# Performance work log

Hardware: AMD Instinct MI355X
Metric: run time of the kernel (lower is better)

The kernel has to match this reference:

```python
import jax, jax.numpy as jnp
import numpy as np

N_SENTS, N_ENTS, BATCH, DIM, HEADS = 64, 16, 64, 512, 8


def setup_inputs() -> dict:
    key = jax.random.key(0)
    ks = jax.random.split(key, 10)
    se = N_SENTS * N_ENTS
    s = 0.02  # init scale for projection weights
    entities = jax.random.normal(ks[0], (se, BATCH, DIM), dtype=jnp.float32)
    query_param = jax.random.uniform(ks[1], (1, 1, DIM), jnp.float32, -1.0, 1.0)
    wq = jax.random.normal(ks[2], (DIM, DIM), jnp.float32) * s
    wk = jax.random.normal(ks[3], (DIM, DIM), jnp.float32) * s
    wv = jax.random.normal(ks[4], (DIM, DIM), jnp.float32) * s
    wo = jax.random.normal(ks[5], (DIM, DIM), jnp.float32) * s
    bq = jax.random.normal(ks[6], (DIM,), jnp.float32) * s
    bk = jax.random.normal(ks[7], (DIM,), jnp.float32) * s
    bv = jax.random.normal(ks[8], (DIM,), jnp.float32) * s
    bo = jax.random.normal(ks[9], (DIM,), jnp.float32) * s
    return {"entities": entities, "query_param": query_param,
            "wq": wq, "wk": wk, "wv": wv, "wo": wo,
            "bq": bq, "bk": bk, "bv": bv, "bo": bo,
            "n_sents": N_SENTS}


def reference(entities, query_param, wq, wk, wv, wo, bq, bk, bv, bo, n_sents):
    # entities: [n_sents*n_ents, batch, dim]
    se, b, d = entities.shape
    n_ents = se // n_sents
    h = HEADS
    hd = d // h

    # Learned single query broadcast to every (sentence, batch) slot.
    q_in = jnp.broadcast_to(query_param, (n_sents, b, d))
    q = q_in @ wq.T + bq            # [n_sents, b, d]
    k = entities @ wk.T + bk        # [se, b, d]
    v = entities @ wv.T + bv        # [se, b, d]

    # Split heads -> [b, h, len, hd]
    qh = q.reshape(n_sents, b, h, hd).transpose(1, 2, 0, 3)
    kh = k.reshape(se, b, h, hd).transpose(1, 2, 0, 3)
    vh = v.reshape(se, b, h, hd).transpose(1, 2, 0, 3)

    scale = jnp.asarray(1.0 / np.sqrt(hd), dtype=qh.dtype)
    scores = jnp.einsum('bhqd,bhkd->bhqk', qh, kh) * scale  # [b,h,n_sents,se]

    # Block-diagonal mask: query i attends only to keys [i*n_ents, (i+1)*n_ents)
    valid = (jnp.arange(se) // n_ents)[None, :] == jnp.arange(n_sents)[:, None]
    scores = jnp.where(valid[None, None], scores, jnp.finfo(scores.dtype).min)

    attn = jax.nn.softmax(scores, axis=-1)
    ctx = jnp.einsum('bhqk,bhkd->bhqd', attn, vh)            # [b,h,n_sents,hd]
    out = ctx.transpose(2, 0, 1, 3).reshape(n_sents, b, d)   # merge heads
    return out @ wo.T + bo                                   # [n_sents, b, d]
```

## Files before the change

kernel.cpp:

```cpp
#include <hip/hip_runtime.h>
#include <stdint.h>

#define HEADS 8
#define DIM   512
#define HD    64
#define NE    16
#define NS    64
#define NB    64

typedef short bf16x8 __attribute__((ext_vector_type(8)));
typedef float f32x4  __attribute__((ext_vector_type(4)));

__device__ __forceinline__ unsigned short f2bf(float f) {
    union { float f; uint32_t u; } v; v.f = f;
    uint32_t u = v.u;
    u += 0x7fffu + ((u >> 16) & 1u);
    return (unsigned short)(u >> 16);
}
__device__ __forceinline__ float bf2f(unsigned short b) {
    union { uint32_t u; float f; } v; v.u = ((uint32_t)b) << 16;
    return v.f;
}

__global__ __launch_bounds__(256) void k_qvec(
    const float* __restrict__ qp, const float* __restrict__ wq,
    const float* __restrict__ bq, float* __restrict__ qvec)
{
    __shared__ float red[32][9];
    const int t = threadIdx.x;
    const int dl = t >> 3, js = t & 7;
    const int d = blockIdx.x * 32 + dl;
    const float* w = wq + (size_t)d * DIM + js * 64;
    const float* q = qp + js * 64;
    float acc = 0.f;
    #pragma unroll 8
    for (int i = 0; i < 64; i++) acc += w[i] * q[i];
    red[dl][js] = acc;
    __syncthreads();
    if (t < 32) {
        float s = 0.f;
        #pragma unroll
        for (int j = 0; j < 8; j++) s += red[t][j];
        const int dd = blockIdx.x * 32 + t;
        qvec[dd] = s + bq[dd];
    }
}

__global__ __launch_bounds__(256) void k_uproj(
    const float* __restrict__ qvec, const float* __restrict__ wk,
    unsigned short* __restrict__ u_bf)
{
    const int h = blockIdx.x;
    const int t = threadIdx.x;
    if (h >= HEADS) {
        ((uint32_t*)u_bf)[h * 256 + t] = 0u;
        return;
    }
    __shared__ float qs[HD];
    if (t < HD) qs[t] = qvec[h * HD + t];
    __syncthreads();
    for (int c = t; c < DIM; c += 256) {
        const float* w = wk + (size_t)(h * HD) * DIM + c;
        float acc = 0.f;
        #pragma unroll 4
        for (int j = 0; j < HD; j++) acc += qs[j] * w[(size_t)j * DIM];
        u_bf[h * DIM + c] = f2bf(acc);
    }
}

__global__ __launch_bounds__(256) void k_attn(
    const float* __restrict__ ents, const unsigned short* __restrict__ u_bf,
    unsigned short* __restrict__ weighted)
{
    __shared__ unsigned short ent_bf[NE * DIM];
    __shared__ float attn_s[NE][16];
    const int t = threadIdx.x;
    const int bid = blockIdx.x;
    const int s = bid >> 6, b = bid & 63;

    {
        const int e = t >> 4, c = t & 15;
        const float* src = ents + ((size_t)(s * NE + e) * NB + b) * DIM;
        const uint32_t swz  = (uint32_t)((e & 7) << 4);
        const uint32_t rowb = (uint32_t)e * (DIM * 2);
        #pragma unroll
        for (int i = 0; i < 8; i++) {
            const int d0 = 4 * c + 64 * i;
            const float4 v = *(const float4*)(src + d0);
            ushort4 hv;
            hv.x = f2bf(v.x); hv.y = f2bf(v.y); hv.z = f2bf(v.z); hv.w = f2bf(v.w);
            *(ushort4*)((char*)ent_bf + ((rowb + (uint32_t)d0 * 2u) ^ swz)) = hv;
        }
    }
    __syncthreads();

    if (t < 64) {
        const int m = t & 15, g = t >> 4;
        const uint32_t aswz = (uint32_t)((m & 7) << 4);
        const uint32_t arow = (uint32_t)m * (DIM * 2);
        const unsigned short* urow = u_bf + m * DIM;
        f32x4 acc = {0.f, 0.f, 0.f, 0.f};
        #pragma unroll
        for (int kk = 0; kk < DIM; kk += 32) {
            const int kp = kk + g * 8;
            bf16x8 af = *(const bf16x8*)((const char*)ent_bf + ((arow + (uint32_t)kp * 2u) ^ aswz));
            bf16x8 bf = *(const bf16x8*)(urow + kp);
            acc = __builtin_amdgcn_mfma_f32_16x16x32_bf16(af, bf, acc, 0, 0, 0);
        }
        const float scale = 0.125f;
        float s0 = acc[0]*scale, s1 = acc[1]*scale, s2 = acc[2]*scale, s3 = acc[3]*scale;
        float mx = fmaxf(fmaxf(s0, s1), fmaxf(s2, s3));
        mx = fmaxf(mx, __shfl_xor(mx, 16));
        mx = fmaxf(mx, __shfl_xor(mx, 32));
        const float p0 = __expf(s0 - mx), p1 = __expf(s1 - mx);
        const float p2 = __expf(s2 - mx), p3 = __expf(s3 - mx);
        float sm = p0 + p1 + p2 + p3;
        sm += __shfl_xor(sm, 16);
        sm += __shfl_xor(sm, 32);
        const float inv = 1.f / sm;
        attn_s[4 * g + 0][m] = p0 * inv;
        attn_s[4 * g + 1][m] = p1 * inv;
        attn_s[4 * g + 2][m] = p2 * inv;
        attn_s[4 * g + 3][m] = p3 * inv;
    }
    __syncthreads();

    float wa[HEADS], wb[HEADS];
    #pragma unroll
    for (int h = 0; h < HEADS; h++) { wa[h] = 0.f; wb[h] = 0.f; }
    const int d0 = 2 * t;
    #pragma unroll
    for (int ee = 0; ee < NE; ee++) {
        const uint32_t off = (((uint32_t)(ee * DIM + d0)) * 2u) ^ ((uint32_t)((ee & 7) << 4));
        const uint32_t pr = *(const uint32_t*)((const char*)ent_bf + off);
        const float v0 = bf2f((unsigned short)(pr & 0xffffu));
        const float v1 = bf2f((unsigned short)(pr >> 16));
        const float4 a0 = *(const float4*)&attn_s[ee][0];
        const float4 a1 = *(const float4*)&attn_s[ee][4];
        wa[0] += a0.x * v0; wb[0] += a0.x * v1;
        wa[1] += a0.y * v0; wb[1] += a0.y * v1;
        wa[2] += a0.z * v0; wb[2] += a0.z * v1;
        wa[3] += a0.w * v0; wb[3] += a0.w * v1;
        wa[4] += a1.x * v0; wb[4] += a1.x * v1;
        wa[5] += a1.y * v0; wb[5] += a1.y * v1;
        wa[6] += a1.z * v0; wb[6] += a1.z * v1;
        wa[7] += a1.w * v0; wb[7] += a1.w * v1;
    }
    unsigned short* wrow = weighted + (size_t)bid * (HEADS * DIM);
    #pragma unroll
    for (int h = 0; h < HEADS; h++) {
        const uint32_t pk = (uint32_t)f2bf(wa[h]) | ((uint32_t)f2bf(wb[h]) << 16);
        *(uint32_t*)(wrow + h * DIM + d0) = pk;
    }
}

template <typename CT>
__global__ __launch_bounds__(256) void k_gemm(
    const unsigned short* __restrict__ A, int lda, int aOffY,
    const float* __restrict__ B, int ldb, int bOffY,
    const float* __restrict__ bias, CT* __restrict__ C, int ldc, int cOffY, int K)
{
    __shared__ unsigned short a_s[64][72];
    __shared__ unsigned short b_s[64][72];
    const int t = threadIdx.x;
    const int m0 = blockIdx.x * 64;
    const int y  = blockIdx.y;
    const int w = t >> 6, l = t & 63;
    const int m = l & 15, g = l >> 4;
    const int lr = t >> 2, lk = (t & 3) * 16;

    const unsigned short* Ap = A + (size_t)(m0 + lr) * lda + (size_t)aOffY * y;
    const float* Bp = B + (size_t)(bOffY * y + lr) * ldb;

    f32x4 acc[4];
    #pragma unroll
    for (int i = 0; i < 4; i++) acc[i] = (f32x4){0.f, 0.f, 0.f, 0.f};

    for (int k0 = 0; k0 < K; k0 += 64) {
        const ushort4 av0 = *(const ushort4*)(Ap + k0 + lk);
        const ushort4 av1 = *(const ushort4*)(Ap + k0 + lk + 4);
        const ushort4 av2 = *(const ushort4*)(Ap + k0 + lk + 8);
        const ushort4 av3 = *(const ushort4*)(Ap + k0 + lk + 12);
        const float4 bv0 = *(const float4*)(Bp + k0 + lk);
        const float4 bv1 = *(const float4*)(Bp + k0 + lk + 4);
        const float4 bv2 = *(const float4*)(Bp + k0 + lk + 8);
        const float4 bv3 = *(const float4*)(Bp + k0 + lk + 12);
        *(ushort4*)&a_s[lr][lk]      = av0;
        *(ushort4*)&a_s[lr][lk + 4]  = av1;
        *(ushort4*)&a_s[lr][lk + 8]  = av2;
        *(ushort4*)&a_s[lr][lk + 12] = av3;
        ushort4 h0, h1, h2, h3;
        h0.x = f2bf(bv0.x); h0.y = f2bf(bv0.y); h0.z = f2bf(bv0.z); h0.w = f2bf(bv0.w);
        h1.x = f2bf(bv1.x); h1.y = f2bf(bv1.y); h1.z = f2bf(bv1.z); h1.w = f2bf(bv1.w);
        h2.x = f2bf(bv2.x); h2.y = f2bf(bv2.y); h2.z = f2bf(bv2.z); h2.w = f2bf(bv2.w);
        h3.x = f2bf(bv3.x); h3.y = f2bf(bv3.y); h3.z = f2bf(bv3.z); h3.w = f2bf(bv3.w);
        *(ushort4*)&b_s[lr][lk]      = h0;
        *(ushort4*)&b_s[lr][lk + 4]  = h1;
        *(ushort4*)&b_s[lr][lk + 8]  = h2;
        *(ushort4*)&b_s[lr][lk + 12] = h3;
        __syncthreads();
        #pragma unroll
        for (int kk = 0; kk < 64; kk += 32) {
            const int kp = kk + g * 8;
            const bf16x8 af = *(const bf16x8*)&a_s[w * 16 + m][kp];
            const bf16x8 b0 = *(const bf16x8*)&b_s[ 0 + m][kp];
            const bf16x8 b1 = *(const bf16x8*)&b_s[16 + m][kp];
            const bf16x8 b2 = *(const bf16x8*)&b_s[32 + m][kp];
            const bf16x8 b3 = *(const bf16x8*)&b_s[48 + m][kp];
            acc[0] = __builtin_amdgcn_mfma_f32_16x16x32_bf16(af, b0, acc[0], 0, 0, 0);
            acc[1] = __builtin_amdgcn_mfma_f32_16x16x32_bf16(af, b1, acc[1], 0, 0, 0);
            acc[2] = __builtin_amdgcn_mfma_f32_16x16x32_bf16(af, b2, acc[2], 0, 0, 0);
            acc[3] = __builtin_amdgcn_mfma_f32_16x16x32_bf16(af, b3, acc[3], 0, 0, 0);
        }
        __syncthreads();
    }

    const int colbase = cOffY * y;
    #pragma unroll
    for (int nt = 0; nt < 4; nt++) {
        const int col = colbase + nt * 16 + m;
        const float bs = bias[col];
        #pragma unroll
        for (int j = 0; j < 4; j++) {
            const int row = m0 + w * 16 + g * 4 + j;
            const float val = acc[nt][j] + bs;
            if (sizeof(CT) == 2) {
                ((unsigned short*)C)[(size_t)row * ldc + col] = f2bf(val);
            } else {
                ((float*)C)[(size_t)row * ldc + col] = val;
            }
        }
    }
}

extern "C" void kernel_launch(void* const* d_in, const int* in_sizes, int n_in,
                              void* d_out, int out_size, void* d_ws, size_t ws_size,
                              hipStream_t stream)
{
    const float* ents = (const float*)d_in[0];
    const float* qp   = (const float*)d_in[1];
    const float* wq   = (const float*)d_in[2];
    const float* wk   = (const float*)d_in[3];
    const float* wv   = (const float*)d_in[4];
    const float* wo   = (const float*)d_in[5];
    const float* bq   = (const float*)d_in[6];
    const float* bv   = (const float*)d_in[8];
    const float* bo   = (const float*)d_in[9];

    char* ws = (char*)d_ws;
    float*          qvec     = (float*)ws;
    unsigned short* u_bf     = (unsigned short*)(ws + 2048);
    unsigned short* weighted = (unsigned short*)(ws + 32768);
    unsigned short* ctx      = (unsigned short*)(ws + 32768 + 33554432);

    k_qvec <<<16, 256, 0, stream>>>(qp, wq, bq, qvec);
    k_uproj<<<16, 256, 0, stream>>>(qvec, wk, u_bf);
    k_attn <<<4096, 256, 0, stream>>>(ents, u_bf, weighted);
    k_gemm<unsigned short><<<dim3(64, 8), 256, 0, stream>>>(
        weighted, HEADS * DIM, DIM, wv, DIM, HD, bv, ctx, DIM, HD, DIM);
    k_gemm<float><<<dim3(64, 8), 256, 0, stream>>>(
        ctx, DIM, 0, wo, DIM, HD, bo, (float*)d_out, DIM, HD, DIM);
}
```

Baseline: 74.67 us.

## Batch four batch slots per attention block and pre-convert weights to bf16

The attention kernel now processes four batch slots per block, so all four wavefronts run the score MFMA instead of one. Each thread also accumulates eight contiguous dims with 16-byte LDS reads and stores. The Wv/Wo fp32 weights are converted to bf16 once in a new prep kernel, removing per-tile conversion in the GEMMs. qvec and u projections are re-split into more, smaller blocks. Costs are a 64KB LDS footprint per attention block, which limits occupancy, and 64 accumulator registers per thread.

```diff
diff --git a/kernel.cpp b/kernel.cpp
--- a/kernel.cpp
+++ b/kernel.cpp
@@ -22,88 +22,100 @@
     return v.f;
 }
 
-__global__ __launch_bounds__(256) void k_qvec(
+__global__ __launch_bounds__(256) void k_prep(
     const float* __restrict__ qp, const float* __restrict__ wq,
-    const float* __restrict__ bq, float* __restrict__ qvec)
-{
-    __shared__ float red[32][9];
+    const float* __restrict__ bq, const float* __restrict__ wv,
+    const float* __restrict__ wo, float* __restrict__ qvec,
+    unsigned short* __restrict__ wv_bf, unsigned short* __restrict__ wo_bf)
+{
+    const int bid = blockIdx.x;
     const int t = threadIdx.x;
-    const int dl = t >> 3, js = t & 7;
-    const int d = blockIdx.x * 32 + dl;
-    const float* w = wq + (size_t)d * DIM + js * 64;
-    const float* q = qp + js * 64;
+    if (bid < 64) {
+        const int dl = t >> 5, js = t & 31;
+        const int d = bid * 8 + dl;
+        const float* w = wq + (size_t)d * DIM + js * 16;
+        const float* q = qp + js * 16;
+        float acc = 0.f;
+        #pragma unroll
+        for (int i = 0; i < 16; i++) acc += w[i] * q[i];
+        #pragma unroll
+        for (int msk = 16; msk >= 1; msk >>= 1) acc += __shfl_xor(acc, msk);
+        if (js == 0) qvec[d] = acc + bq[d];
+        return;
+    }
+    const bool is_v = bid < 320;
+    const float* src = is_v ? wv : wo;
+    unsigned short* dst = is_v ? wv_bf : wo_bf;
+    const int li = ((is_v ? bid - 64 : bid - 320) * 1024 + t * 4);
+    const float4 v = *(const float4*)(src + li);
+    ushort4 hv;
+    hv.x = f2bf(v.x); hv.y = f2bf(v.y); hv.z = f2bf(v.z); hv.w = f2bf(v.w);
+    *(ushort4*)(dst + li) = hv;
+}
+
+__global__ __launch_bounds__(64) void k_uproj(
+    const float* __restrict__ qvec, const float* __restrict__ wk,
+    unsigned short* __restrict__ u_bf)
+{
+    const int bid = blockIdx.x;
+    const int l = threadIdx.x;
+    if (bid >= 64) {
+        const int row = 8 + (bid - 64);
+        ((uint4*)(u_bf + row * DIM))[l & 63] = (uint4){0u, 0u, 0u, 0u};
+        return;
+    }
+    const int h = bid >> 3, cg = bid & 7;
+    __shared__ float qs[HD];
+    qs[l] = qvec[h * HD + l];
+    __syncthreads();
+    const int c = cg * 64 + l;
+    const float* w = wk + (size_t)(h * HD) * DIM + c;
     float acc = 0.f;
     #pragma unroll 8
-    for (int i = 0; i < 64; i++) acc += w[i] * q[i];
-    red[dl][js] = acc;
-    __syncthreads();
-    if (t < 32) {
-        float s = 0.f;
-        #pragma unroll
-        for (int j = 0; j < 8; j++) s += red[t][j];
-        const int dd = blockIdx.x * 32 + t;
-        qvec[dd] = s + bq[dd];
-    }
-}
-
-__global__ __launch_bounds__(256) void k_uproj(
-    const float* __restrict__ qvec, const float* __restrict__ wk,
-    unsigned short* __restrict__ u_bf)
-{
-    const int h = blockIdx.x;
-    const int t = threadIdx.x;
-    if (h >= HEADS) {
-        ((uint32_t*)u_bf)[h * 256 + t] = 0u;
-        return;
-    }
-    __shared__ float qs[HD];
-    if (t < HD) qs[t] = qvec[h * HD + t];
-    __syncthreads();
-    for (int c = t; c < DIM; c += 256) {
-        const float* w = wk + (size_t)(h * HD) * DIM + c;
-        float acc = 0.f;
-        #pragma unroll 4
-        for (int j = 0; j < HD; j++) acc += qs[j] * w[(size_t)j * DIM];
-        u_bf[h * DIM + c] = f2bf(acc);
-    }
-}
-
-__global__ __launch_bounds__(256) void k_attn(
+    for (int j = 0; j < HD; j++) acc += qs[j] * w[(size_t)j * DIM];
+    u_bf[h * DIM + c] = f2bf(acc);
+}
+
+__global__ __launch_bounds__(256, 2) void k_attn(
     const float* __restrict__ ents, const unsigned short* __restrict__ u_bf,
     unsigned short* __restrict__ weighted)
 {
-    __shared__ unsigned short ent_bf[NE * DIM];
-    __shared__ float attn_s[NE][16];
+    __shared__ unsigned short ent[NE * 4 * DIM];
+    __shared__ float attn_s[4][NE][16];
     const int t = threadIdx.x;
     const int bid = blockIdx.x;
-    const int s = bid >> 6, b = bid & 63;
+    const int s = bid >> 4;
+    const int bg = (bid & 15) << 2;
 
     {
-        const int e = t >> 4, c = t & 15;
-        const float* src = ents + ((size_t)(s * NE + e) * NB + b) * DIM;
-        const uint32_t swz  = (uint32_t)((e & 7) << 4);
-        const uint32_t rowb = (uint32_t)e * (DIM * 2);
-        #pragma unroll
-        for (int i = 0; i < 8; i++) {
-            const int d0 = 4 * c + 64 * i;
-            const float4 v = *(const float4*)(src + d0);
+        const float* base = ents + ((size_t)(s * NE) * NB + bg) * DIM;
+        #pragma unroll 4
+        for (int i = 0; i < 32; i++) {
+            const int li = t + 256 * i;
+            const int e  = li >> 9;
+            const int bb = (li >> 7) & 3;
+            const int d0 = (li & 127) << 2;
+            const float4 v = *(const float4*)(base + ((size_t)e * NB + bb) * DIM + d0);
             ushort4 hv;
             hv.x = f2bf(v.x); hv.y = f2bf(v.y); hv.z = f2bf(v.z); hv.w = f2bf(v.w);
-            *(ushort4*)((char*)ent_bf + ((rowb + (uint32_t)d0 * 2u) ^ swz)) = hv;
+            const uint32_t off = (uint32_t)((((e * 4 + bb) << 9) + d0) << 1) ^ (uint32_t)((e & 7) << 4);
+            *(ushort4*)((char*)ent + off) = hv;
         }
     }
     __syncthreads();
 
-    if (t < 64) {
-        const int m = t & 15, g = t >> 4;
+    const int w = t >> 6, l = t & 63;
+    const int m = l & 15, g = l >> 4;
+
+    {
         const uint32_t aswz = (uint32_t)((m & 7) << 4);
-        const uint32_t arow = (uint32_t)m * (DIM * 2);
+        const uint32_t abase = (uint32_t)((m * 4 + w) << 10);
         const unsigned short* urow = u_bf + m * DIM;
         f32x4 acc = {0.f, 0.f, 0.f, 0.f};
         #pragma unroll
         for (int kk = 0; kk < DIM; kk += 32) {
             const int kp = kk + g * 8;
-            bf16x8 af = *(const bf16x8*)((const char*)ent_bf + ((arow + (uint32_t)kp * 2u) ^ aswz));
+            bf16x8 af = *(const bf16x8*)((const char*)ent + ((abase + (uint32_t)(kp << 1)) ^ aswz));
             bf16x8 bf = *(const bf16x8*)(urow + kp);
             acc = __builtin_amdgcn_mfma_f32_16x16x32_bf16(af, bf, acc, 0, 0, 0);
         }
@@ -118,46 +130,50 @@
         sm += __shfl_xor(sm, 16);
         sm += __shfl_xor(sm, 32);
         const float inv = 1.f / sm;
-        attn_s[4 * g + 0][m] = p0 * inv;
-        attn_s[4 * g + 1][m] = p1 * inv;
-        attn_s[4 * g + 2][m] = p2 * inv;
-        attn_s[4 * g + 3][m] = p3 * inv;
+        attn_s[w][4 * g + 0][m] = p0 * inv;
+        attn_s[w][4 * g + 1][m] = p1 * inv;
+        attn_s[w][4 * g + 2][m] = p2 * inv;
+        attn_s[w][4 * g + 3][m] = p3 * inv;
     }
     __syncthreads();
 
-    float wa[HEADS], wb[HEADS];
-    #pragma unroll
-    for (int h = 0; h < HEADS; h++) { wa[h] = 0.f; wb[h] = 0.f; }
-    const int d0 = 2 * t;
-    #pragma unroll
-    for (int ee = 0; ee < NE; ee++) {
-        const uint32_t off = (((uint32_t)(ee * DIM + d0)) * 2u) ^ ((uint32_t)((ee & 7) << 4));
-        const uint32_t pr = *(const uint32_t*)((const char*)ent_bf + off);
-        const float v0 = bf2f((unsigned short)(pr & 0xffffu));
-        const float v1 = bf2f((unsigned short)(pr >> 16));
-        const float4 a0 = *(const float4*)&attn_s[ee][0];
-        const float4 a1 = *(const float4*)&attn_s[ee][4];
-        wa[0] += a0.x * v0; wb[0] += a0.x * v1;
-        wa[1] += a0.y * v0; wb[1] += a0.y * v1;
-        wa[2] += a0.z * v0; wb[2] += a0.z * v1;
-        wa[3] += a0.w * v0; wb[3] += a0.w * v1;
-        wa[4] += a1.x * v0; wb[4] += a1.x * v1;
-        wa[5] += a1.y * v0; wb[5] += a1.y * v1;
-        wa[6] += a1.z * v0; wb[6] += a1.z * v1;
-        wa[7] += a1.w * v0; wb[7] += a1.w * v1;
-    }
-    unsigned short* wrow = weighted + (size_t)bid * (HEADS * DIM);
+    float acc2[HEADS][8];
+    #pragma unroll
+    for (int h = 0; h < HEADS; h++)
+        #pragma unroll
+        for (int j = 0; j < 8; j++) acc2[h][j] = 0.f;
+
+    const int d0 = l << 3;
+    #pragma unroll
+    for (int e = 0; e < NE; e++) {
+        const uint32_t off = (uint32_t)((((e * 4 + w) << 9) + d0) << 1) ^ (uint32_t)((e & 7) << 4);
+        const bf16x8 ev = *(const bf16x8*)((const char*)ent + off);
+        const unsigned short* ep = (const unsigned short*)&ev;
+        float evf[8];
+        #pragma unroll
+        for (int j = 0; j < 8; j++) evf[j] = bf2f(ep[j]);
+        const float4 a0 = *(const float4*)&attn_s[w][e][0];
+        const float4 a1 = *(const float4*)&attn_s[w][e][4];
+        float av[8] = {a0.x, a0.y, a0.z, a0.w, a1.x, a1.y, a1.z, a1.w};
+        #pragma unroll
+        for (int h = 0; h < HEADS; h++)
+            #pragma unroll
+            for (int j = 0; j < 8; j++) acc2[h][j] += av[h] * evf[j];
+    }
+    unsigned short* wrow = weighted + ((size_t)(s * NB + bg + w) << 12);
     #pragma unroll
     for (int h = 0; h < HEADS; h++) {
-        const uint32_t pk = (uint32_t)f2bf(wa[h]) | ((uint32_t)f2bf(wb[h]) << 16);
-        *(uint32_t*)(wrow + h * DIM + d0) = pk;
+        bf16x8 ov;
+        #pragma unroll
+        for (int j = 0; j < 8; j++) ov[j] = (short)f2bf(acc2[h][j]);
+        *(bf16x8*)(wrow + h * DIM + d0) = ov;
     }
 }
 
 template <typename CT>
 __global__ __launch_bounds__(256) void k_gemm(
     const unsigned short* __restrict__ A, int lda, int aOffY,
-    const float* __restrict__ B, int ldb, int bOffY,
+    const unsigned short* __restrict__ B, int ldb, int bOffY,
     const float* __restrict__ bias, CT* __restrict__ C, int ldc, int cOffY, int K)
 {
     __shared__ unsigned short a_s[64][72];
@@ -170,7 +186,7 @@
     const int lr = t >> 2, lk = (t & 3) * 16;
 
     const unsigned short* Ap = A + (size_t)(m0 + lr) * lda + (size_t)aOffY * y;
-    const float* Bp = B + (size_t)(bOffY * y + lr) * ldb;
+    const unsigned short* Bp = B + (size_t)(bOffY * y + lr) * ldb;
 
     f32x4 acc[4];
     #pragma unroll
@@ -181,23 +197,18 @@
         const ushort4 av1 = *(const ushort4*)(Ap + k0 + lk + 4);
         const ushort4 av2 = *(const ushort4*)(Ap + k0 + lk + 8);
         const ushort4 av3 = *(const ushort4*)(Ap + k0 + lk + 12);
-        const float4 bv0 = *(const float4*)(Bp + k0 + lk);
-        const float4 bv1 = *(const float4*)(Bp + k0 + lk + 4);
-        const float4 bv2 = *(const float4*)(Bp + k0 + lk + 8);
-        const float4 bv3 = *(const float4*)(Bp + k0 + lk + 12);
+        const ushort4 bv0 = *(const ushort4*)(Bp + k0 + lk);
+        const ushort4 bv1 = *(const ushort4*)(Bp + k0 + lk + 4);
+        const ushort4 bv2 = *(const ushort4*)(Bp + k0 + lk + 8);
+        const ushort4 bv3 = *(const ushort4*)(Bp + k0 + lk + 12);
         *(ushort4*)&a_s[lr][lk]      = av0;
         *(ushort4*)&a_s[lr][lk + 4]  = av1;
         *(ushort4*)&a_s[lr][lk + 8]  = av2;
         *(ushort4*)&a_s[lr][lk + 12] = av3;
-        ushort4 h0, h1, h2, h3;
-        h0.x = f2bf(bv0.x); h0.y = f2bf(bv0.y); h0.z = f2bf(bv0.z); h0.w = f2bf(bv0.w);
-        h1.x = f2bf(bv1.x); h1.y = f2bf(bv1.y); h1.z = f2bf(bv1.z); h1.w = f2bf(bv1.w);
-        h2.x = f2bf(bv2.x); h2.y = f2bf(bv2.y); h2.z = f2bf(bv2.z); h2.w = f2bf(bv2.w);
-        h3.x = f2bf(bv3.x); h3.y = f2bf(bv3.y); h3.z = f2bf(bv3.z); h3.w = f2bf(bv3.w);
-        *(ushort4*)&b_s[lr][lk]      = h0;
-        *(ushort4*)&b_s[lr][lk + 4]  = h1;
-        *(ushort4*)&b_s[lr][lk + 8]  = h2;
-        *(ushort4*)&b_s[lr][lk + 12] = h3;
+        *(ushort4*)&b_s[lr][lk]      = bv0;
+        *(ushort4*)&b_s[lr][lk + 4]  = bv1;
+        *(ushort4*)&b_s[lr][lk + 8]  = bv2;
+        *(ushort4*)&b_s[lr][lk + 12] = bv3;
         __syncthreads();
         #pragma unroll
         for (int kk = 0; kk < 64; kk += 32) {
@@ -249,15 +260,17 @@
 
     char* ws = (char*)d_ws;
     float*          qvec     = (float*)ws;
-    unsigned short* u_bf     = (unsigned short*)(ws + 2048);
-    unsigned short* weighted = (unsigned short*)(ws + 32768);
-    unsigned short* ctx      = (unsigned short*)(ws + 32768 + 33554432);
-
-    k_qvec <<<16, 256, 0, stream>>>(qp, wq, bq, qvec);
-    k_uproj<<<16, 256, 0, stream>>>(qvec, wk, u_bf);
-    k_attn <<<4096, 256, 0, stream>>>(ents, u_bf, weighted);
+    unsigned short* u_bf     = (unsigned short*)(ws + 4096);
+    unsigned short* wv_bf    = (unsigned short*)(ws + 65536);
+    unsigned short* wo_bf    = (unsigned short*)(ws + 65536 + 524288);
+    unsigned short* weighted = (unsigned short*)(ws + 2097152);
+    unsigned short* ctx      = (unsigned short*)(ws + 2097152 + 33554432);
+
+    k_prep <<<576, 256, 0, stream>>>(qp, wq, bq, wv, wo, qvec, wv_bf, wo_bf);
+    k_uproj<<<72, 64, 0, stream>>>(qvec, wk, u_bf);
+    k_attn <<<1024, 256, 0, stream>>>(ents, u_bf, weighted);
     k_gemm<unsigned short><<<dim3(64, 8), 256, 0, stream>>>(
-        weighted, HEADS * DIM, DIM, wv, DIM, HD, bv, ctx, DIM, HD, DIM);
+        weighted, HEADS * DIM, DIM, wv_bf, DIM, HD, bv, ctx, DIM, HD, DIM);
     k_gemm<float><<<dim3(64, 8), 256, 0, stream>>>(
-        ctx, DIM, 0, wo, DIM, HD, bo, (float*)d_out, DIM, HD, DIM);
-}
+        ctx, DIM, 0, wo_bf, DIM, HD, bo, (float*)d_out, DIM, HD, DIM);
+}
```

Result: faster. 68.30 us (-8.5%).
